# Kernel optimization log

Hardware: AMD Instinct MI355X
Metric: run time of the kernel (lower is better)

Reference implementation:

```python
import jax, jax.numpy as jnp
import numpy as np

EPS_NORM = 1e-12   # F.normalize eps
EPS_DIST = 1e-4    # sqrt stabilizer from original code
EPSILON = 1e-8     # log stabilizer (forward default arg)


def setup_inputs() -> dict:
    key = jax.random.key(0)
    thought_vectors = jax.random.normal(key, (4, 2048, 1024), dtype=jnp.float32)
    return {"thought_vectors": thought_vectors}


def reference(thought_vectors):
    # NOTE: original code casts to fp32 then discards it by re-reshaping the
    # raw input; inputs here are already fp32 so the math is identical.
    D = thought_vectors.shape[-1]
    x = thought_vectors.reshape(-1, D)                          # [N, D]
    norm = jnp.linalg.norm(x, axis=-1, keepdims=True)
    x = x / jnp.maximum(norm, EPS_NORM)                         # L2 normalize
    N = x.shape[0]
    sim = jnp.minimum(jnp.einsum('nd,md->nm', x, x), 1.0)       # [N, N], clamp max=1
    dists = jnp.sqrt(2.0 - 2.0 * sim + EPS_DIST)                # chordal distance
    dists = jnp.where(jnp.eye(N, dtype=bool), jnp.inf, dists)   # mask self
    min_dist = jnp.min(dists, axis=1)                           # nearest neighbor
    return -jnp.mean(jnp.log(min_dist + EPSILON))
```

## Files before the change

### kernel.cpp

```cpp
#include <hip/hip_runtime.h>
#include <hip/hip_bf16.h>
#include <math.h>

#define N_ROWS 8192
#define DIM    1024
#define NB     (N_ROWS / 128)
#define NT     (NB * (NB + 1) / 2)

typedef __bf16 bf16_t;
typedef __bf16 bf16x4 __attribute__((ext_vector_type(4)));
typedef __bf16 bf16x8 __attribute__((ext_vector_type(8)));
typedef float  f32x4  __attribute__((ext_vector_type(4)));

#define GLOAD_LDS(g, s) __builtin_amdgcn_global_load_lds(                      \
    (const __attribute__((address_space(1))) void*)(g),                        \
    (__attribute__((address_space(3))) void*)(s), 16, 0, 0)

__device__ __forceinline__ unsigned fmap(float f) {
    unsigned u = __float_as_uint(f);
    return (u & 0x80000000u) ? ~u : (u | 0x80000000u);
}
__device__ __forceinline__ float funmap(unsigned u) {
    return (u & 0x80000000u) ? __uint_as_float(u ^ 0x80000000u)
                             : __uint_as_float(~u);
}

__global__ __launch_bounds__(256) void k_normalize(const float* __restrict__ x,
                                                   bf16_t* __restrict__ xb,
                                                   unsigned* __restrict__ row_max) {
    const int tid = threadIdx.x;
    const int l   = tid & 63;
    const int row = blockIdx.x * 4 + (tid >> 6);
    const float4* xr = reinterpret_cast<const float4*>(x + (size_t)row * DIM);

    float4 v[4];
    float ss = 0.0f;
    #pragma unroll
    for (int c = 0; c < 4; ++c) {
        v[c] = xr[l + c * 64];
        ss += v[c].x * v[c].x + v[c].y * v[c].y + v[c].z * v[c].z + v[c].w * v[c].w;
    }
    #pragma unroll
    for (int m = 32; m >= 1; m >>= 1) ss += __shfl_xor(ss, m);
    const float scale = 1.0f / fmaxf(sqrtf(ss), 1e-12f);

    bf16x4* xo = reinterpret_cast<bf16x4*>(xb + (size_t)row * DIM);
    #pragma unroll
    for (int c = 0; c < 4; ++c) {
        bf16x4 o;
        o[0] = (bf16_t)(v[c].x * scale);
        o[1] = (bf16_t)(v[c].y * scale);
        o[2] = (bf16_t)(v[c].z * scale);
        o[3] = (bf16_t)(v[c].w * scale);
        xo[l + c * 64] = o;
    }

    if (blockIdx.x < N_ROWS / 256)
        row_max[blockIdx.x * 256 + tid] = 0u;
}

__global__ __launch_bounds__(256) void k_simmax(const bf16_t* __restrict__ xb,
                                                unsigned* __restrict__ row_max) {
    __shared__ bf16_t smA[128 * 64];
    __shared__ bf16_t smB[128 * 64];
    const int tid = threadIdx.x;
    const int w  = tid >> 6;
    const int l  = tid & 63;
    const int lr = l & 15;
    const int lk = (l >> 4) * 8;
    const int wr = w >> 1, wc = w & 1;

    int t = blockIdx.x;
    #define TOFF(b) ((b) * NB - ((b) * ((b) - 1)) / 2)
    int bi = (int)((float)(2 * NB + 1 -
                sqrtf((float)((2 * NB + 1) * (2 * NB + 1) - 8 * t))) * 0.5f);
    if (bi < 0) bi = 0;
    if (bi > NB - 1) bi = NB - 1;
    while (TOFF(bi + 1) <= t) ++bi;
    while (TOFF(bi) > t) --bi;
    const int bj = bi + (t - TOFF(bi));
    const int i0 = bi * 128, j0 = bj * 128;

    const int srow = tid >> 3, schk = (tid & 7) * 8;
    const bf16_t* gA = xb + (size_t)(i0 + srow) * DIM + schk;
    const bf16_t* gB = xb + (size_t)(j0 + srow) * DIM + schk;
    const int wbase = (tid & ~63) * 8;

    f32x4 acc[4][4] = {};
    const bf16_t* pa = smA + (wr * 64 + lr) * 64 + lk;
    const bf16_t* pb = smB + (wc * 64 + lr) * 64 + lk;

    for (int k = 0; k < DIM; k += 64) {
        #pragma unroll
        for (int q = 0; q < 4; ++q) {
            GLOAD_LDS(gA + (size_t)(q * 32) * DIM + k, smA + q * 2048 + wbase);
            GLOAD_LDS(gB + (size_t)(q * 32) * DIM + k, smB + q * 2048 + wbase);
        }
        __syncthreads();

        #pragma unroll
        for (int ks = 0; ks < 2; ++ks) {
            bf16x8 af[4], bfr[4];
            #pragma unroll
            for (int m = 0; m < 4; ++m)
                af[m]  = *(const bf16x8*)(pa + m * 1024 + ks * 32);
            #pragma unroll
            for (int n = 0; n < 4; ++n)
                bfr[n] = *(const bf16x8*)(pb + n * 1024 + ks * 32);
            #pragma unroll
            for (int m = 0; m < 4; ++m)
                #pragma unroll
                for (int n = 0; n < 4; ++n)
                    acc[m][n] = __builtin_amdgcn_mfma_f32_16x16x32_bf16(
                                    af[m], bfr[n], acc[m][n], 0, 0, 0);
        }
        __syncthreads();
    }

    #pragma unroll
    for (int m = 0; m < 4; ++m) {
        #pragma unroll
        for (int j = 0; j < 4; ++j) {
            const int rowg = i0 + wr * 64 + m * 16 + (l >> 4) * 4 + j;
            float rm = -3.0e38f;
            #pragma unroll
            for (int n = 0; n < 4; ++n) {
                float s = acc[m][n][j];
                if (rowg == (j0 + wc * 64 + n * 16 + lr)) s = -3.0e38f;
                rm = fmaxf(rm, s);
            }
            #pragma unroll
            for (int mask = 1; mask < 16; mask <<= 1)
                rm = fmaxf(rm, __shfl_xor(rm, mask));
            if (lr == 0)
                atomicMax(&row_max[rowg], fmap(fminf(rm, 1.0f)));
        }
    }
    if (bi != bj) {
        #pragma unroll
        for (int n = 0; n < 4; ++n) {
            const int colg = j0 + wc * 64 + n * 16 + lr;
            float cm = -3.0e38f;
            #pragma unroll
            for (int m = 0; m < 4; ++m)
                #pragma unroll
                for (int j = 0; j < 4; ++j)
                    cm = fmaxf(cm, acc[m][n][j]);
            cm = fmaxf(cm, __shfl_xor(cm, 16));
            cm = fmaxf(cm, __shfl_xor(cm, 32));
            if (l < 16)
                atomicMax(&row_max[colg], fmap(fminf(cm, 1.0f)));
        }
    }
}

__global__ __launch_bounds__(1024) void k_finish(const unsigned* __restrict__ row_max,
                                                 float* __restrict__ out) {
    const int tid = threadIdx.x;
    float sum = 0.0f;
    #pragma unroll
    for (int i = tid; i < N_ROWS; i += 1024) {
        float sim = fminf(funmap(row_max[i]), 1.0f);
        float dist = sqrtf(2.0f - 2.0f * sim + 1e-4f);
        sum += logf(dist + 1e-8f);
    }
    #pragma unroll
    for (int m = 32; m >= 1; m >>= 1) sum += __shfl_xor(sum, m);
    __shared__ float wss[16];
    if ((tid & 63) == 0) wss[tid >> 6] = sum;
    __syncthreads();
    if (tid == 0) {
        float tot = 0.0f;
        #pragma unroll
        for (int i = 0; i < 16; ++i) tot += wss[i];
        out[0] = -tot / (float)N_ROWS;
    }
}

extern "C" void kernel_launch(void* const* d_in, const int* in_sizes, int n_in,
                              void* d_out, int out_size, void* d_ws, size_t ws_size,
                              hipStream_t stream) {
    const float* x = (const float*)d_in[0];
    bf16_t* xb = (bf16_t*)d_ws;
    unsigned* row_max = (unsigned*)((char*)d_ws +
                         (size_t)N_ROWS * DIM * sizeof(bf16_t));
    float* out = (float*)d_out;

    k_normalize<<<N_ROWS / 4, 256, 0, stream>>>(x, xb, row_max);
    k_simmax<<<NT, 256, 0, stream>>>(xb, row_max);
    k_finish<<<1, 1024, 0, stream>>>(row_max, out);
}
```

Measured before the change: 210.9 us.

## Double-buffer LDS k-loop and fold final reduction into simmax via last-block counter

The GEMM main loop now uses two 32-wide K stages in LDS and prefetches the next stage while computing the current one, so global-to-LDS loads overlap with MFMA work instead of sitting behind a barrier. The separate finish kernel is removed: each tile block increments a global counter and the last one to finish computes the log-mean over row maxima. This removes one kernel launch. In exchange it adds an atomic per block and a serial tail in one block, and it halves the K depth per barrier.

```diff
diff --git a/kernel.cpp b/kernel.cpp
--- a/kernel.cpp
+++ b/kernel.cpp
@@ -27,7 +27,8 @@
 
 __global__ __launch_bounds__(256) void k_normalize(const float* __restrict__ x,
                                                    bf16_t* __restrict__ xb,
-                                                   unsigned* __restrict__ row_max) {
+                                                   unsigned* __restrict__ row_max,
+                                                   unsigned* __restrict__ counter) {
     const int tid = threadIdx.x;
     const int l   = tid & 63;
     const int row = blockIdx.x * 4 + (tid >> 6);
@@ -57,12 +58,15 @@
 
     if (blockIdx.x < N_ROWS / 256)
         row_max[blockIdx.x * 256 + tid] = 0u;
+    if (blockIdx.x == 0 && tid == 0) counter[0] = 0u;
 }
 
 __global__ __launch_bounds__(256) void k_simmax(const bf16_t* __restrict__ xb,
-                                                unsigned* __restrict__ row_max) {
-    __shared__ bf16_t smA[128 * 64];
-    __shared__ bf16_t smB[128 * 64];
+                                                unsigned* __restrict__ row_max,
+                                                unsigned* __restrict__ counter,
+                                                float* __restrict__ out) {
+    __shared__ bf16_t smA0[128 * 32], smA1[128 * 32];
+    __shared__ bf16_t smB0[128 * 32], smB1[128 * 32];
     const int tid = threadIdx.x;
     const int w  = tid >> 6;
     const int l  = tid & 63;
@@ -81,40 +85,50 @@
     const int bj = bi + (t - TOFF(bi));
     const int i0 = bi * 128, j0 = bj * 128;
 
-    const int srow = tid >> 3, schk = (tid & 7) * 8;
-    const bf16_t* gA = xb + (size_t)(i0 + srow) * DIM + schk;
-    const bf16_t* gB = xb + (size_t)(j0 + srow) * DIM + schk;
+    const bf16_t* gA = xb + (size_t)(i0 + (tid >> 2)) * DIM + (tid & 3) * 8;
+    const bf16_t* gB = xb + (size_t)(j0 + (tid >> 2)) * DIM + (tid & 3) * 8;
     const int wbase = (tid & ~63) * 8;
 
+    #define STAGE(sa, sb, kk) do {                                             \
+        GLOAD_LDS(gA + (kk),            (sa) + wbase);                         \
+        GLOAD_LDS(gA + 64 * DIM + (kk), (sa) + 2048 + wbase);                  \
+        GLOAD_LDS(gB + (kk),            (sb) + wbase);                         \
+        GLOAD_LDS(gB + 64 * DIM + (kk), (sb) + 2048 + wbase);                  \
+    } while (0)
+
     f32x4 acc[4][4] = {};
-    const bf16_t* pa = smA + (wr * 64 + lr) * 64 + lk;
-    const bf16_t* pb = smB + (wc * 64 + lr) * 64 + lk;
-
-    for (int k = 0; k < DIM; k += 64) {
-        #pragma unroll
-        for (int q = 0; q < 4; ++q) {
-            GLOAD_LDS(gA + (size_t)(q * 32) * DIM + k, smA + q * 2048 + wbase);
-            GLOAD_LDS(gB + (size_t)(q * 32) * DIM + k, smB + q * 2048 + wbase);
-        }
-        __syncthreads();
-
-        #pragma unroll
-        for (int ks = 0; ks < 2; ++ks) {
-            bf16x8 af[4], bfr[4];
-            #pragma unroll
-            for (int m = 0; m < 4; ++m)
-                af[m]  = *(const bf16x8*)(pa + m * 1024 + ks * 32);
-            #pragma unroll
-            for (int n = 0; n < 4; ++n)
-                bfr[n] = *(const bf16x8*)(pb + n * 1024 + ks * 32);
-            #pragma unroll
-            for (int m = 0; m < 4; ++m)
-                #pragma unroll
-                for (int n = 0; n < 4; ++n)
-                    acc[m][n] = __builtin_amdgcn_mfma_f32_16x16x32_bf16(
-                                    af[m], bfr[n], acc[m][n], 0, 0, 0);
-        }
-        __syncthreads();
+    const int fa = (wr * 64 + lr) * 32 + lk;
+    const int fb = (wc * 64 + lr) * 32 + lk;
+
+    #define COMPUTE(sa, sb) do {                                               \
+        bf16x8 af[4], bfr[4];                                                  \
+        _Pragma("unroll")                                                      \
+        for (int m = 0; m < 4; ++m) af[m]  = *(const bf16x8*)((sa) + fa + m * 512); \
+        _Pragma("unroll")                                                      \
+        for (int n = 0; n < 4; ++n) bfr[n] = *(const bf16x8*)((sb) + fb + n * 512); \
+        _Pragma("unroll")                                                      \
+        for (int m = 0; m < 4; ++m)                                            \
+            _Pragma("unroll")                                                  \
+            for (int n = 0; n < 4; ++n)                                        \
+                acc[m][n] = __builtin_amdgcn_mfma_f32_16x16x32_bf16(           \
+                                af[m], bfr[n], acc[m][n], 0, 0, 0);            \
+    } while (0)
+
+    STAGE(smA0, smB0, 0);
+    __syncthreads();
+    for (int k = 0; k < DIM - 64; k += 64) {
+        STAGE(smA1, smB1, k + 32);
+        COMPUTE(smA0, smB0);
+        __syncthreads();
+        STAGE(smA0, smB0, k + 64);
+        COMPUTE(smA1, smB1);
+        __syncthreads();
+    }
+    {
+        STAGE(smA1, smB1, DIM - 32);
+        COMPUTE(smA0, smB0);
+        __syncthreads();
+        COMPUTE(smA1, smB1);
     }
 
     #pragma unroll
@@ -152,28 +166,29 @@
                 atomicMax(&row_max[colg], fmap(fminf(cm, 1.0f)));
         }
     }
-}
-
-__global__ __launch_bounds__(1024) void k_finish(const unsigned* __restrict__ row_max,
-                                                 float* __restrict__ out) {
-    const int tid = threadIdx.x;
-    float sum = 0.0f;
-    #pragma unroll
-    for (int i = tid; i < N_ROWS; i += 1024) {
-        float sim = fminf(funmap(row_max[i]), 1.0f);
-        float dist = sqrtf(2.0f - 2.0f * sim + 1e-4f);
-        sum += logf(dist + 1e-8f);
-    }
-    #pragma unroll
-    for (int m = 32; m >= 1; m >>= 1) sum += __shfl_xor(sum, m);
-    __shared__ float wss[16];
-    if ((tid & 63) == 0) wss[tid >> 6] = sum;
+
     __syncthreads();
+    __shared__ unsigned slast;
     if (tid == 0) {
-        float tot = 0.0f;
+        __threadfence();
+        slast = (atomicAdd(counter, 1u) == NT - 1) ? 1u : 0u;
+    }
+    __syncthreads();
+    if (slast) {
+        float sum = 0.0f;
+        for (int i = tid; i < N_ROWS; i += 256) {
+            unsigned u = atomicMax(&row_max[i], 0u);
+            float sim = fminf(funmap(u), 1.0f);
+            float dist = sqrtf(2.0f - 2.0f * sim + 1e-4f);
+            sum += logf(dist + 1e-8f);
+        }
         #pragma unroll
-        for (int i = 0; i < 16; ++i) tot += wss[i];
-        out[0] = -tot / (float)N_ROWS;
+        for (int m = 32; m >= 1; m >>= 1) sum += __shfl_xor(sum, m);
+        __shared__ float wss[4];
+        if ((tid & 63) == 0) wss[tid >> 6] = sum;
+        __syncthreads();
+        if (tid == 0)
+            out[0] = -(wss[0] + wss[1] + wss[2] + wss[3]) / (float)N_ROWS;
     }
 }
 
@@ -184,9 +199,9 @@
     bf16_t* xb = (bf16_t*)d_ws;
     unsigned* row_max = (unsigned*)((char*)d_ws +
                          (size_t)N_ROWS * DIM * sizeof(bf16_t));
+    unsigned* counter = row_max + N_ROWS;
     float* out = (float*)d_out;
 
-    k_normalize<<<N_ROWS / 4, 256, 0, stream>>>(x, xb, row_max);
-    k_simmax<<<NT, 256, 0, stream>>>(xb, row_max);
-    k_finish<<<1, 1024, 0, stream>>>(row_max, out);
-}
+    k_normalize<<<N_ROWS / 4, 256, 0, stream>>>(x, xb, row_max, counter);
+    k_simmax<<<NT, 256, 0, stream>>>(xb, row_max, counter, out);
+}
```

New measurement: 240.0 us. 1.14x slower.
